# Optimization experiments

Measured on AMD Instinct MI355X. Metric: run time of the kernel, lower is better.

Reference implementation:

```python
import jax, jax.numpy as jnp
import numpy as np

EMBED_DIM = 1024
NUM_HEADS = 16
HEAD_DIM = EMBED_DIM // NUM_HEADS
LN_EPS = 1e-5


def setup_inputs() -> dict:
    key = jax.random.key(0)
    ks = jax.random.split(key, 10)
    B, S, D = 1, 4096, EMBED_DIM
    s = 1.0 / np.sqrt(D)
    inp = {
        'input': jax.random.normal(ks[0], (B, S, D), dtype=jnp.float32),
        'Wq': jax.random.normal(ks[1], (D, D), dtype=jnp.float32) * s,
        'bq': jnp.zeros((D,), dtype=jnp.float32),
        'Wk': jax.random.normal(ks[2], (D, D), dtype=jnp.float32) * s,
        'bk': jnp.zeros((D,), dtype=jnp.float32),
        'Wv': jax.random.normal(ks[3], (D, D), dtype=jnp.float32) * s,
        'bv': jnp.zeros((D,), dtype=jnp.float32),
        'Wo': jax.random.normal(ks[4], (D, D), dtype=jnp.float32) * s,
        'bo': jnp.zeros((D,), dtype=jnp.float32),
        'ln_gamma': jnp.ones((D,), dtype=jnp.float32),
        'ln_beta': jnp.zeros((D,), dtype=jnp.float32),
    }
    return inp


def reference(input, Wq, bq, Wk, bk, Wv, bv, Wo, bo, ln_gamma, ln_beta):
    B, S, D = input.shape
    H, Hd = NUM_HEADS, HEAD_DIM
    # projections (torch Linear: x @ W.T + b)
    q = input @ Wq.T + bq
    k = input @ Wk.T + bk
    v = input @ Wv.T + bv
    # [B, H, S, Hd]
    q = q.reshape(B, S, H, Hd).transpose(0, 2, 1, 3)
    k = k.reshape(B, S, H, Hd).transpose(0, 2, 1, 3)
    v = v.reshape(B, S, H, Hd).transpose(0, 2, 1, 3)
    scores = jnp.einsum('bhqd,bhkd->bhqk', q, k) / jnp.sqrt(jnp.float32(Hd))
    causal = jnp.tril(jnp.ones((S, S), dtype=bool))  # [S, S]
    scores = jnp.where(causal[None, None, :, :], scores, -jnp.inf)
    attn = jax.nn.softmax(scores, axis=-1)  # stable (max-subtract) internally
    out = jnp.einsum('bhqk,bhkd->bhqd', attn, v)
    out = out.transpose(0, 2, 1, 3).reshape(B, S, D)
    out = out @ Wo.T + bo
    out = out + input
    # LayerNorm
    mu = jnp.mean(out, axis=-1, keepdims=True)
    var = jnp.var(out, axis=-1, keepdims=True)
    normed = (out - mu) * jax.lax.rsqrt(var + LN_EPS)
    return normed * ln_gamma + ln_beta
```

## Files before the change

kernel.cpp:

```cpp
#include <hip/hip_runtime.h>
#include <hip/hip_bf16.h>

typedef float floatx4 __attribute__((ext_vector_type(4)));
typedef short short8 __attribute__((ext_vector_type(8)));

#define S_LEN 4096
#define D_DIM 1024
#define NHEAD 16
#define SCALE_LOG2 0.1803368801111204f

__device__ __forceinline__ void gload_lds16(const void* g, void* l) {
  __builtin_amdgcn_global_load_lds(
      (const __attribute__((address_space(1))) unsigned int*)g,
      (__attribute__((address_space(3))) unsigned int*)l, 16, 0, 0);
}

__device__ __forceinline__ unsigned short f2bf_bits(float f) {
  __hip_bfloat16 h = __float2bfloat16(f);
  return __builtin_bit_cast(unsigned short, h);
}

__global__ __launch_bounds__(256) void cvt_all(const float* __restrict__ x,
                                               const float* __restrict__ w0,
                                               const float* __restrict__ w1,
                                               const float* __restrict__ w2,
                                               const float* __restrict__ w3,
                                               unsigned short* __restrict__ xo,
                                               unsigned short* __restrict__ o0,
                                               unsigned short* __restrict__ o1,
                                               unsigned short* __restrict__ o2,
                                               unsigned short* __restrict__ o3) {
  const int bid = blockIdx.x;
  const float* in;
  unsigned short* out;
  int i;
  if (bid < 4096) {
    in = x;
    out = xo;
    i = bid * 256 + threadIdx.x;
  } else {
    const int which = (bid - 4096) >> 10;
    in = which == 0 ? w0 : which == 1 ? w1 : which == 2 ? w2 : w3;
    out = which == 0 ? o0 : which == 1 ? o1 : which == 2 ? o2 : o3;
    i = ((bid - 4096) & 1023) * 256 + threadIdx.x;
  }
  float4 v = reinterpret_cast<const float4*>(in)[i];
  ushort4 u;
  u.x = f2bf_bits(v.x);
  u.y = f2bf_bits(v.y);
  u.z = f2bf_bits(v.z);
  u.w = f2bf_bits(v.w);
  reinterpret_cast<ushort4*>(out)[i] = u;
}

__global__ __launch_bounds__(256) void gemm_qkv(const unsigned short* __restrict__ A,
                                                const unsigned short* __restrict__ WqB,
                                                const unsigned short* __restrict__ WkB,
                                                const unsigned short* __restrict__ WvB,
                                                const float* __restrict__ bq,
                                                const float* __restrict__ bk,
                                                const float* __restrict__ bv,
                                                unsigned short* __restrict__ Qo,
                                                unsigned short* __restrict__ Ko,
                                                unsigned short* __restrict__ VTo) {
  __shared__ __align__(16) unsigned short As[128 * 32];
  __shared__ __align__(16) unsigned short Bs[128 * 32];
  const int K = 1024, N = 1024, M = 4096;
  const int tid = threadIdx.x;
  const int wave = tid >> 6, lane = tid & 63;
  const int seg = blockIdx.y >> 3;
  const int m0 = blockIdx.x * 128, n0 = (blockIdx.y & 7) * 128;
  const unsigned short* B = seg == 0 ? WqB : seg == 1 ? WkB : WvB;
  const float* bias = seg == 0 ? bq : seg == 1 ? bk : bv;
  const int wr = wave >> 1, wc = wave & 1;

  floatx4 acc[4][4] = {};
  const unsigned short* Ab = A + (size_t)m0 * K;
  const unsigned short* Bb = B + (size_t)n0 * K;
  const int srow = lane >> 2, scol = (lane & 3) * 8;
  const int aRow = lane & 15, kOff = (lane >> 4) * 8;

  for (int k0 = 0; k0 < K; k0 += 32) {
#pragma unroll
    for (int i = 0; i < 2; ++i) {
      const int c = wave * 2 + i;
      const int row = c * 16 + srow;
      gload_lds16(Ab + (size_t)row * K + k0 + scol, &As[c * 512]);
      gload_lds16(Bb + (size_t)row * K + k0 + scol, &Bs[c * 512]);
    }
    __syncthreads();
    short8 af[4], bfg[4];
#pragma unroll
    for (int f = 0; f < 4; ++f) {
      af[f] = *reinterpret_cast<const short8*>(&As[(wr * 64 + f * 16 + aRow) * 32 + kOff]);
      bfg[f] = *reinterpret_cast<const short8*>(&Bs[(wc * 64 + f * 16 + aRow) * 32 + kOff]);
    }
#pragma unroll
    for (int fm = 0; fm < 4; ++fm)
#pragma unroll
      for (int fn = 0; fn < 4; ++fn)
        acc[fm][fn] =
            __builtin_amdgcn_mfma_f32_16x16x32_bf16(af[fm], bfg[fn], acc[fm][fn], 0, 0, 0);
    __syncthreads();
  }

  const int rb = (lane >> 4) * 4, cl = lane & 15;
  const float osc = seg == 0 ? SCALE_LOG2 : 1.0f;
#pragma unroll
  for (int fm = 0; fm < 4; ++fm)
#pragma unroll
    for (int fn = 0; fn < 4; ++fn)
#pragma unroll
      for (int r = 0; r < 4; ++r) {
        const int row = m0 + wr * 64 + fm * 16 + rb + r;
        const int col = n0 + wc * 64 + fn * 16 + cl;
        const float v = (acc[fm][fn][r] + bias[col]) * osc;
        if (seg == 0)
          Qo[(size_t)row * N + col] = f2bf_bits(v);
        else if (seg == 1)
          Ko[(size_t)row * N + col] = f2bf_bits(v);
        else
          VTo[(size_t)col * M + row] = f2bf_bits(v);
      }
}

__global__ __launch_bounds__(256) void gemm_o(const unsigned short* __restrict__ A,
                                              const unsigned short* __restrict__ B,
                                              const float* __restrict__ bias,
                                              const float* __restrict__ resid,
                                              float* __restrict__ C) {
  __shared__ __align__(16) unsigned short As[64 * 32];
  __shared__ __align__(16) unsigned short Bs[128 * 32];
  const int K = 1024, N = 1024;
  const int tid = threadIdx.x;
  const int wave = tid >> 6, lane = tid & 63;
  const int m0 = blockIdx.x * 64, n0 = blockIdx.y * 128;
  const int wr = wave >> 1, wc = wave & 1;

  floatx4 acc[2][4] = {};
  const unsigned short* Ab = A + (size_t)m0 * K;
  const unsigned short* Bb = B + (size_t)n0 * K;
  const int srow = lane >> 2, scol = (lane & 3) * 8;
  const int aRow = lane & 15, kOff = (lane >> 4) * 8;

  for (int k0 = 0; k0 < K; k0 += 32) {
#pragma unroll
    for (int i = 0; i < 3; ++i) {
      const int ci = wave * 3 + i;
      if (ci < 4) {
        const int row = ci * 16 + srow;
        gload_lds16(Ab + (size_t)row * K + k0 + scol, &As[ci * 512]);
      } else {
        const int row = (ci - 4) * 16 + srow;
        gload_lds16(Bb + (size_t)row * K + k0 + scol, &Bs[(ci - 4) * 512]);
      }
    }
    __syncthreads();
    short8 af[2], bfg[4];
#pragma unroll
    for (int f = 0; f < 2; ++f)
      af[f] = *reinterpret_cast<const short8*>(&As[(wr * 32 + f * 16 + aRow) * 32 + kOff]);
#pragma unroll
    for (int f = 0; f < 4; ++f)
      bfg[f] = *reinterpret_cast<const short8*>(&Bs[(wc * 64 + f * 16 + aRow) * 32 + kOff]);
#pragma unroll
    for (int fm = 0; fm < 2; ++fm)
#pragma unroll
      for (int fn = 0; fn < 4; ++fn)
        acc[fm][fn] =
            __builtin_amdgcn_mfma_f32_16x16x32_bf16(af[fm], bfg[fn], acc[fm][fn], 0, 0, 0);
    __syncthreads();
  }

  const int rb = (lane >> 4) * 4, cl = lane & 15;
#pragma unroll
  for (int fm = 0; fm < 2; ++fm)
#pragma unroll
    for (int fn = 0; fn < 4; ++fn)
#pragma unroll
      for (int r = 0; r < 4; ++r) {
        const int row = m0 + wr * 32 + fm * 16 + rb + r;
        const int col = n0 + wc * 64 + fn * 16 + cl;
        C[(size_t)row * N + col] =
            acc[fm][fn][r] + bias[col] + resid[(size_t)row * N + col];
      }
}

__global__ __launch_bounds__(256) void attn_fwd(const unsigned short* __restrict__ Q,
                                                const unsigned short* __restrict__ Kg,
                                                const unsigned short* __restrict__ VT,
                                                unsigned short* __restrict__ O) {
  __shared__ __align__(16) unsigned short Ks[2 * 64 * 64];
  __shared__ __align__(16) unsigned short Vs[2 * 64 * 64];
  __shared__ __align__(16) unsigned short Ps[4][16 * 64];

  const int bid = blockIdx.x;
  const int h = bid & 15;
  const int qt = 63 - (bid >> 4);
  const int q0 = qt * 64;
  const int wave = threadIdx.x >> 6, lane = threadIdx.x & 63;
  const int l15 = lane & 15, l4 = lane >> 4;
  const int q7 = l15 & 7;

  const int qrow = q0 + wave * 16 + l15;
  short8 qf[2];
#pragma unroll
  for (int ks = 0; ks < 2; ++ks)
    qf[ks] = *reinterpret_cast<const short8*>(
        &Q[(size_t)qrow * D_DIM + h * 64 + ks * 32 + l4 * 8]);

  floatx4 acco[4] = {};
  float l_run = 0.f;

  auto stage = [&](int buf, int t) {
    const int kv0 = t * 64;
#pragma unroll
    for (int i = 0; i < 2; ++i) {
      const int seg = wave * 2 + i;
      const int c = seg * 64 + lane;
      const int r = c >> 3, jj = c & 7;
      const int sj = (jj ^ (r & 7)) * 8;
      gload_lds16(&Kg[(size_t)(kv0 + r) * D_DIM + h * 64 + sj],
                  &Ks[buf * 4096 + seg * 512]);
      gload_lds16(&VT[(size_t)(h * 64 + r) * S_LEN + kv0 + sj],
                  &Vs[buf * 4096 + seg * 512]);
    }
  };

  const int ntiles = qt + 1;
  stage(0, 0);
  int cur = 0;
  for (int t = 0; t < ntiles; ++t) {
    if (t + 1 < ntiles) {
      stage(cur ^ 1, t + 1);
      asm volatile("s_waitcnt vmcnt(4)" ::: "memory");
    } else {
      asm volatile("s_waitcnt vmcnt(0)" ::: "memory");
    }
    __builtin_amdgcn_s_barrier();

    const unsigned short* ksb = &Ks[cur * 4096];
    const unsigned short* vsb = &Vs[cur * 4096];
    const int kv0 = t * 64;

    floatx4 accs[4] = {};
#pragma unroll
    for (int ks = 0; ks < 2; ++ks)
#pragma unroll
      for (int fn = 0; fn < 4; ++fn) {
        const int R = fn * 16 + l15;
        const int J = ks * 4 + l4;
        const short8 kf =
            *reinterpret_cast<const short8*>(&ksb[R * 64 + ((J ^ (R & 7)) * 8)]);
        accs[fn] =
            __builtin_amdgcn_mfma_f32_16x16x32_bf16(kf, qf[ks], accs[fn], 0, 0, 0);
      }

    float p[4][4];
    if (t == ntiles - 1) {
#pragma unroll
      for (int fn = 0; fn < 4; ++fn)
#pragma unroll
        for (int r = 0; r < 4; ++r) {
          const int ka = kv0 + fn * 16 + l4 * 4 + r;
          const float s = (ka > qrow) ? -1e30f : accs[fn][r];
          p[fn][r] = __builtin_amdgcn_exp2f(s);
        }
    } else {
#pragma unroll
      for (int fn = 0; fn < 4; ++fn)
#pragma unroll
        for (int r = 0; r < 4; ++r) p[fn][r] = __builtin_amdgcn_exp2f(accs[fn][r]);
    }
    float rs = 0.f;
#pragma unroll
    for (int fn = 0; fn < 4; ++fn)
#pragma unroll
      for (int r = 0; r < 4; ++r) rs += p[fn][r];
    l_run += rs;

#pragma unroll
    for (int fn = 0; fn < 4; ++fn) {
      const int c = 2 * fn + (l4 >> 1);
      const int off = ((c ^ q7) << 3) + ((l4 & 1) << 2);
      uint2 w;
      w.x = (unsigned)f2bf_bits(p[fn][0]) | ((unsigned)f2bf_bits(p[fn][1]) << 16);
      w.y = (unsigned)f2bf_bits(p[fn][2]) | ((unsigned)f2bf_bits(p[fn][3]) << 16);
      *reinterpret_cast<uint2*>(&Ps[wave][l15 * 64 + off]) = w;
    }

#pragma unroll
    for (int kh = 0; kh < 2; ++kh) {
      const short8 pf = *reinterpret_cast<const short8*>(
          &Ps[wave][l15 * 64 + (((kh * 4 + l4) ^ q7) << 3)]);
#pragma unroll
      for (int fn = 0; fn < 4; ++fn) {
        const int R = fn * 16 + l15;
        const int J = kh * 4 + l4;
        const short8 vf =
            *reinterpret_cast<const short8*>(&vsb[R * 64 + ((J ^ (R & 7)) * 8)]);
        acco[fn] = __builtin_amdgcn_mfma_f32_16x16x32_bf16(vf, pf, acco[fn], 0, 0, 0);
      }
    }
    __builtin_amdgcn_s_barrier();
    cur ^= 1;
  }

  l_run += __shfl_xor(l_run, 16);
  l_run += __shfl_xor(l_run, 32);
  const float inv = 1.f / l_run;
#pragma unroll
  for (int fn = 0; fn < 4; ++fn)
#pragma unroll
    for (int rp = 0; rp < 2; ++rp) {
      const unsigned lo = f2bf_bits(acco[fn][2 * rp] * inv);
      const unsigned hi = f2bf_bits(acco[fn][2 * rp + 1] * inv);
      *reinterpret_cast<unsigned*>(
          &O[(size_t)qrow * D_DIM + h * 64 + fn * 16 + l4 * 4 + rp * 2]) =
          lo | (hi << 16);
    }
}

__global__ __launch_bounds__(256) void ln_kernel(const float* __restrict__ X,
                                                 const float* __restrict__ g,
                                                 const float* __restrict__ b,
                                                 float* __restrict__ Y) {
  const int row = blockIdx.x;
  const int t = threadIdx.x;
  const float4 xv = reinterpret_cast<const float4*>(X + (size_t)row * 1024)[t];
  float s = xv.x + xv.y + xv.z + xv.w;
  float s2 = xv.x * xv.x + xv.y * xv.y + xv.z * xv.z + xv.w * xv.w;
#pragma unroll
  for (int off = 1; off < 64; off <<= 1) {
    s += __shfl_xor(s, off);
    s2 += __shfl_xor(s2, off);
  }
  __shared__ float sr[4], sr2[4];
  const int wave = t >> 6, lane = t & 63;
  if (lane == 0) {
    sr[wave] = s;
    sr2[wave] = s2;
  }
  __syncthreads();
  const float S = sr[0] + sr[1] + sr[2] + sr[3];
  const float S2 = sr2[0] + sr2[1] + sr2[2] + sr2[3];
  const float mu = S * (1.f / 1024.f);
  const float var = S2 * (1.f / 1024.f) - mu * mu;
  const float rstd = rsqrtf(var + 1e-5f);
  const float4 gv = reinterpret_cast<const float4*>(g)[t];
  const float4 bv = reinterpret_cast<const float4*>(b)[t];
  float4 y;
  y.x = (xv.x - mu) * rstd * gv.x + bv.x;
  y.y = (xv.y - mu) * rstd * gv.y + bv.y;
  y.z = (xv.z - mu) * rstd * gv.z + bv.z;
  y.w = (xv.w - mu) * rstd * gv.w + bv.w;
  reinterpret_cast<float4*>(Y + (size_t)row * 1024)[t] = y;
}

extern "C" void kernel_launch(void* const* d_in, const int* in_sizes, int n_in,
                              void* d_out, int out_size, void* d_ws, size_t ws_size,
                              hipStream_t stream) {
  const float* x = (const float*)d_in[0];
  const float* Wq = (const float*)d_in[1];
  const float* bq = (const float*)d_in[2];
  const float* Wk = (const float*)d_in[3];
  const float* bk = (const float*)d_in[4];
  const float* Wv = (const float*)d_in[5];
  const float* bv = (const float*)d_in[6];
  const float* Wo = (const float*)d_in[7];
  const float* bo = (const float*)d_in[8];
  const float* gamma = (const float*)d_in[9];
  const float* beta = (const float*)d_in[10];

  char* ws = (char*)d_ws;
  const size_t MB = (size_t)1 << 20;
  unsigned short* Xb = (unsigned short*)(ws + 0);
  unsigned short* Wqb = (unsigned short*)(ws + 8 * MB);
  unsigned short* Wkb = (unsigned short*)(ws + 10 * MB);
  unsigned short* Wvb = (unsigned short*)(ws + 12 * MB);
  unsigned short* Wob = (unsigned short*)(ws + 16 * MB);
  unsigned short* Qb = (unsigned short*)(ws + 18 * MB);
  unsigned short* Kb = (unsigned short*)(ws + 26 * MB);
  unsigned short* VTb = (unsigned short*)(ws + 34 * MB);
  unsigned short* Ab = (unsigned short*)(ws + 42 * MB);
  float* proj = (float*)(ws + 0);

  cvt_all<<<8192, 256, 0, stream>>>(x, Wq, Wk, Wv, Wo, Xb, Wqb, Wkb, Wvb, Wob);

  gemm_qkv<<<dim3(32, 24), 256, 0, stream>>>(Xb, Wqb, Wkb, Wvb, bq, bk, bv, Qb, Kb,
                                             VTb);

  attn_fwd<<<dim3(1024), 256, 0, stream>>>(Qb, Kb, VTb, Ab);

  gemm_o<<<dim3(64, 8), 256, 0, stream>>>(Ab, Wob, bo, x, proj);

  ln_kernel<<<4096, 256, 0, stream>>>(proj, gamma, beta, (float*)d_out);
}
```

Baseline: 146.9 us.

## Double K-tile depth with XOR-swizzled LDS and transposed MFMA for V output

```diff
diff --git a/kernel.cpp b/kernel.cpp
--- a/kernel.cpp
+++ b/kernel.cpp
@@ -63,8 +63,8 @@
                                                 unsigned short* __restrict__ Qo,
                                                 unsigned short* __restrict__ Ko,
                                                 unsigned short* __restrict__ VTo) {
-  __shared__ __align__(16) unsigned short As[128 * 32];
-  __shared__ __align__(16) unsigned short Bs[128 * 32];
+  __shared__ __align__(16) unsigned short As[128 * 64];
+  __shared__ __align__(16) unsigned short Bs[128 * 64];
   const int K = 1024, N = 1024, M = 4096;
   const int tid = threadIdx.x;
   const int wave = tid >> 6, lane = tid & 63;
@@ -77,51 +77,76 @@
   floatx4 acc[4][4] = {};
   const unsigned short* Ab = A + (size_t)m0 * K;
   const unsigned short* Bb = B + (size_t)n0 * K;
-  const int srow = lane >> 2, scol = (lane & 3) * 8;
-  const int aRow = lane & 15, kOff = (lane >> 4) * 8;
-
-  for (int k0 = 0; k0 < K; k0 += 32) {
-#pragma unroll
-    for (int i = 0; i < 2; ++i) {
-      const int c = wave * 2 + i;
-      const int row = c * 16 + srow;
-      gload_lds16(Ab + (size_t)row * K + k0 + scol, &As[c * 512]);
-      gload_lds16(Bb + (size_t)row * K + k0 + scol, &Bs[c * 512]);
+  const int srow = lane >> 3;
+  const int sj = ((lane & 7) ^ (srow & 7)) * 8;
+  const int aRow = lane & 15, l4 = lane >> 4;
+
+  for (int k0 = 0; k0 < K; k0 += 64) {
+#pragma unroll
+    for (int i = 0; i < 4; ++i) {
+      const int c = wave * 4 + i;
+      const int row = c * 8 + srow;
+      gload_lds16(Ab + (size_t)row * K + k0 + sj, &As[c * 512]);
+      gload_lds16(Bb + (size_t)row * K + k0 + sj, &Bs[c * 512]);
     }
     __syncthreads();
-    short8 af[4], bfg[4];
-#pragma unroll
-    for (int f = 0; f < 4; ++f) {
-      af[f] = *reinterpret_cast<const short8*>(&As[(wr * 64 + f * 16 + aRow) * 32 + kOff]);
-      bfg[f] = *reinterpret_cast<const short8*>(&Bs[(wc * 64 + f * 16 + aRow) * 32 + kOff]);
-    }
+#pragma unroll
+    for (int kk = 0; kk < 2; ++kk) {
+      short8 af[4], bfg[4];
+#pragma unroll
+      for (int f = 0; f < 4; ++f) {
+        const int ra = wr * 64 + f * 16 + aRow;
+        const int rb2 = wc * 64 + f * 16 + aRow;
+        af[f] = *reinterpret_cast<const short8*>(
+            &As[ra * 64 + (((kk * 4 + l4) ^ (ra & 7)) * 8)]);
+        bfg[f] = *reinterpret_cast<const short8*>(
+            &Bs[rb2 * 64 + (((kk * 4 + l4) ^ (rb2 & 7)) * 8)]);
+      }
+      if (seg == 2) {
+#pragma unroll
+        for (int fm = 0; fm < 4; ++fm)
+#pragma unroll
+          for (int fn = 0; fn < 4; ++fn)
+            acc[fm][fn] = __builtin_amdgcn_mfma_f32_16x16x32_bf16(bfg[fn], af[fm],
+                                                                  acc[fm][fn], 0, 0, 0);
+      } else {
+#pragma unroll
+        for (int fm = 0; fm < 4; ++fm)
+#pragma unroll
+          for (int fn = 0; fn < 4; ++fn)
+            acc[fm][fn] = __builtin_amdgcn_mfma_f32_16x16x32_bf16(af[fm], bfg[fn],
+                                                                  acc[fm][fn], 0, 0, 0);
+      }
+    }
+    __syncthreads();
+  }
+
+  const int rb = (lane >> 4) * 4, cl = lane & 15;
+  if (seg == 2) {
 #pragma unroll
     for (int fm = 0; fm < 4; ++fm)
 #pragma unroll
       for (int fn = 0; fn < 4; ++fn)
-        acc[fm][fn] =
-            __builtin_amdgcn_mfma_f32_16x16x32_bf16(af[fm], bfg[fn], acc[fm][fn], 0, 0, 0);
-    __syncthreads();
-  }
-
-  const int rb = (lane >> 4) * 4, cl = lane & 15;
-  const float osc = seg == 0 ? SCALE_LOG2 : 1.0f;
-#pragma unroll
-  for (int fm = 0; fm < 4; ++fm)
-#pragma unroll
-    for (int fn = 0; fn < 4; ++fn)
-#pragma unroll
-      for (int r = 0; r < 4; ++r) {
-        const int row = m0 + wr * 64 + fm * 16 + rb + r;
-        const int col = n0 + wc * 64 + fn * 16 + cl;
-        const float v = (acc[fm][fn][r] + bias[col]) * osc;
-        if (seg == 0)
-          Qo[(size_t)row * N + col] = f2bf_bits(v);
-        else if (seg == 1)
-          Ko[(size_t)row * N + col] = f2bf_bits(v);
-        else
-          VTo[(size_t)col * M + row] = f2bf_bits(v);
-      }
+#pragma unroll
+        for (int r = 0; r < 4; ++r) {
+          const int n = n0 + wc * 64 + fn * 16 + rb + r;
+          const int m = m0 + wr * 64 + fm * 16 + cl;
+          VTo[(size_t)n * M + m] = f2bf_bits(acc[fm][fn][r] + bias[n]);
+        }
+  } else {
+    const float osc = seg == 0 ? SCALE_LOG2 : 1.0f;
+    unsigned short* Co = seg == 0 ? Qo : Ko;
+#pragma unroll
+    for (int fm = 0; fm < 4; ++fm)
+#pragma unroll
+      for (int fn = 0; fn < 4; ++fn)
+#pragma unroll
+        for (int r = 0; r < 4; ++r) {
+          const int row = m0 + wr * 64 + fm * 16 + rb + r;
+          const int col = n0 + wc * 64 + fn * 16 + cl;
+          Co[(size_t)row * N + col] = f2bf_bits((acc[fm][fn][r] + bias[col]) * osc);
+        }
+  }
 }
 
 __global__ __launch_bounds__(256) void gemm_o(const unsigned short* __restrict__ A,
@@ -129,8 +154,8 @@
                                               const float* __restrict__ bias,
                                               const float* __restrict__ resid,
                                               float* __restrict__ C) {
-  __shared__ __align__(16) unsigned short As[64 * 32];
-  __shared__ __align__(16) unsigned short Bs[128 * 32];
+  __shared__ __align__(16) unsigned short As[64 * 64];
+  __shared__ __align__(16) unsigned short Bs[128 * 64];
   const int K = 1024, N = 1024;
   const int tid = threadIdx.x;
   const int wave = tid >> 6, lane = tid & 63;
@@ -140,35 +165,45 @@
   floatx4 acc[2][4] = {};
   const unsigned short* Ab = A + (size_t)m0 * K;
   const unsigned short* Bb = B + (size_t)n0 * K;
-  const int srow = lane >> 2, scol = (lane & 3) * 8;
-  const int aRow = lane & 15, kOff = (lane >> 4) * 8;
-
-  for (int k0 = 0; k0 < K; k0 += 32) {
-#pragma unroll
-    for (int i = 0; i < 3; ++i) {
-      const int ci = wave * 3 + i;
-      if (ci < 4) {
-        const int row = ci * 16 + srow;
-        gload_lds16(Ab + (size_t)row * K + k0 + scol, &As[ci * 512]);
+  const int srow = lane >> 3;
+  const int sj = ((lane & 7) ^ (srow & 7)) * 8;
+  const int aRow = lane & 15, l4 = lane >> 4;
+
+  for (int k0 = 0; k0 < K; k0 += 64) {
+#pragma unroll
+    for (int i = 0; i < 6; ++i) {
+      const int ci = wave * 6 + i;
+      if (ci < 8) {
+        const int row = ci * 8 + srow;
+        gload_lds16(Ab + (size_t)row * K + k0 + sj, &As[ci * 512]);
       } else {
-        const int row = (ci - 4) * 16 + srow;
-        gload_lds16(Bb + (size_t)row * K + k0 + scol, &Bs[(ci - 4) * 512]);
+        const int row = (ci - 8) * 8 + srow;
+        gload_lds16(Bb + (size_t)row * K + k0 + sj, &Bs[(ci - 8) * 512]);
       }
     }
     __syncthreads();
-    short8 af[2], bfg[4];
-#pragma unroll
-    for (int f = 0; f < 2; ++f)
-      af[f] = *reinterpret_cast<const short8*>(&As[(wr * 32 + f * 16 + aRow) * 32 + kOff]);
-#pragma unroll
-    for (int f = 0; f < 4; ++f)
-      bfg[f] = *reinterpret_cast<const short8*>(&Bs[(wc * 64 + f * 16 + aRow) * 32 + kOff]);
-#pragma unroll
-    for (int fm = 0; fm < 2; ++fm)
-#pragma unroll
-      for (int fn = 0; fn < 4; ++fn)
-        acc[fm][fn] =
-            __builtin_amdgcn_mfma_f32_16x16x32_bf16(af[fm], bfg[fn], acc[fm][fn], 0, 0, 0);
+#pragma unroll
+    for (int kk = 0; kk < 2; ++kk) {
+      short8 af[2], bfg[4];
+#pragma unroll
+      for (int f = 0; f < 2; ++f) {
+        const int ra = wr * 32 + f * 16 + aRow;
+        af[f] = *reinterpret_cast<const short8*>(
+            &As[ra * 64 + (((kk * 4 + l4) ^ (ra & 7)) * 8)]);
+      }
+#pragma unroll
+      for (int f = 0; f < 4; ++f) {
+        const int rb2 = wc * 64 + f * 16 + aRow;
+        bfg[f] = *reinterpret_cast<const short8*>(
+            &Bs[rb2 * 64 + (((kk * 4 + l4) ^ (rb2 & 7)) * 8)]);
+      }
+#pragma unroll
+      for (int fm = 0; fm < 2; ++fm)
+#pragma unroll
+        for (int fn = 0; fn < 4; ++fn)
+          acc[fm][fn] = __builtin_amdgcn_mfma_f32_16x16x32_bf16(af[fm], bfg[fn],
+                                                                acc[fm][fn], 0, 0, 0);
+    }
     __syncthreads();
   }
 
```

Result: slower. 157.2 us (+7.1%).

## Software-pipeline attention loop so P@V of previous tile overlaps current QK

Applied to the files above, without the earlier changes.

```diff
diff --git a/kernel.cpp b/kernel.cpp
--- a/kernel.cpp
+++ b/kernel.cpp
@@ -212,7 +212,7 @@
   floatx4 acco[4] = {};
   float l_run = 0.f;
 
-  auto stage = [&](int buf, int t) {
+  auto stageK = [&](int buf, int t) {
     const int kv0 = t * 64;
 #pragma unroll
     for (int i = 0; i < 2; ++i) {
@@ -222,26 +222,31 @@
       const int sj = (jj ^ (r & 7)) * 8;
       gload_lds16(&Kg[(size_t)(kv0 + r) * D_DIM + h * 64 + sj],
                   &Ks[buf * 4096 + seg * 512]);
+    }
+  };
+  auto stageV = [&](int buf, int t) {
+    const int kv0 = t * 64;
+#pragma unroll
+    for (int i = 0; i < 2; ++i) {
+      const int seg = wave * 2 + i;
+      const int c = seg * 64 + lane;
+      const int r = c >> 3, jj = c & 7;
+      const int sj = (jj ^ (r & 7)) * 8;
       gload_lds16(&VT[(size_t)(h * 64 + r) * S_LEN + kv0 + sj],
                   &Vs[buf * 4096 + seg * 512]);
     }
   };
 
   const int ntiles = qt + 1;
-  stage(0, 0);
-  int cur = 0;
+  stageK(0, 0);
+
   for (int t = 0; t < ntiles; ++t) {
-    if (t + 1 < ntiles) {
-      stage(cur ^ 1, t + 1);
-      asm volatile("s_waitcnt vmcnt(4)" ::: "memory");
-    } else {
-      asm volatile("s_waitcnt vmcnt(0)" ::: "memory");
-    }
+    asm volatile("s_waitcnt vmcnt(0)" ::: "memory");
     __builtin_amdgcn_s_barrier();
-
-    const unsigned short* ksb = &Ks[cur * 4096];
-    const unsigned short* vsb = &Vs[cur * 4096];
-    const int kv0 = t * 64;
+    if (t + 1 < ntiles) stageK((t + 1) & 1, t + 1);
+    stageV(t & 1, t);
+
+    const unsigned short* ksb = &Ks[(t & 1) * 4096];
 
     floatx4 accs[4] = {};
 #pragma unroll
@@ -256,6 +261,24 @@
             __builtin_amdgcn_mfma_f32_16x16x32_bf16(kf, qf[ks], accs[fn], 0, 0, 0);
       }
 
+    if (t > 0) {
+      const unsigned short* vsb = &Vs[((t - 1) & 1) * 4096];
+#pragma unroll
+      for (int kh = 0; kh < 2; ++kh) {
+        const short8 pf = *reinterpret_cast<const short8*>(
+            &Ps[wave][l15 * 64 + (((kh * 4 + l4) ^ q7) << 3)]);
+#pragma unroll
+        for (int fn = 0; fn < 4; ++fn) {
+          const int R = fn * 16 + l15;
+          const int J = kh * 4 + l4;
+          const short8 vf =
+              *reinterpret_cast<const short8*>(&vsb[R * 64 + ((J ^ (R & 7)) * 8)]);
+          acco[fn] = __builtin_amdgcn_mfma_f32_16x16x32_bf16(vf, pf, acco[fn], 0, 0, 0);
+        }
+      }
+    }
+
+    const int kv0 = t * 64;
     float p[4][4];
     if (t == ntiles - 1) {
 #pragma unroll
@@ -288,7 +311,12 @@
       w.y = (unsigned)f2bf_bits(p[fn][2]) | ((unsigned)f2bf_bits(p[fn][3]) << 16);
       *reinterpret_cast<uint2*>(&Ps[wave][l15 * 64 + off]) = w;
     }
-
+  }
+
+  asm volatile("s_waitcnt vmcnt(0)" ::: "memory");
+  __builtin_amdgcn_s_barrier();
+  {
+    const unsigned short* vsb = &Vs[((ntiles - 1) & 1) * 4096];
 #pragma unroll
     for (int kh = 0; kh < 2; ++kh) {
       const short8 pf = *reinterpret_cast<const short8*>(
@@ -302,8 +330,6 @@
         acco[fn] = __builtin_amdgcn_mfma_f32_16x16x32_bf16(vf, pf, acco[fn], 0, 0, 0);
       }
     }
-    __builtin_amdgcn_s_barrier();
-    cur ^= 1;
   }
 
   l_run += __shfl_xor(l_run, 16);
```

Result: faster. 142.8 us (-2.8%).
